# Kernel tuning notes

Measured on AMD Instinct MI355X. Metric: run time of the kernel, lower is better.

## Reference

```python
import jax, jax.numpy as jnp
import numpy as np

B, S, F, H = 2, 2048, 2048, 16
DH = F // H  # head_dim = 128
ROPE_BASE = 10000.0


def apply_rope(x, offset):
    # x: [B, S, H, Dh]; rotate-half RoPE per head with positions offset..offset+S-1
    d = x.shape[-1]
    pos = jnp.arange(x.shape[1], dtype=jnp.float32) + offset          # [S]
    inv_freq = 1.0 / (ROPE_BASE ** (jnp.arange(0, d, 2, dtype=jnp.float32) / d))  # [Dh/2]
    ang = pos[:, None] * inv_freq[None, :]                             # [S, Dh/2]
    cos = jnp.cos(ang)[None, :, None, :].astype(x.dtype)               # [1,S,1,Dh/2]
    sin = jnp.sin(ang)[None, :, None, :].astype(x.dtype)
    x1, x2 = x[..., : d // 2], x[..., d // 2 :]
    return jnp.concatenate([x1 * cos - x2 * sin, x1 * sin + x2 * cos], axis=-1)


def setup_inputs() -> dict:
    key = jax.random.key(0)
    k0, k1, k2, k3 = jax.random.split(key, 4)
    lecun = (1.0 / F) ** 0.5
    in_q = jax.random.normal(k0, (B, S, F), dtype=jnp.float32)
    Wq = jax.random.normal(k1, (F, H, DH), dtype=jnp.float32) * lecun
    Wk = jax.random.normal(k2, (F, H, DH), dtype=jnp.float32) * lecun
    Wv = jax.random.normal(k3, (F, H, DH), dtype=jnp.float32) * lecun
    bq = jnp.zeros((H, DH), dtype=jnp.float32)
    bk = jnp.zeros((H, DH), dtype=jnp.float32)
    bv = jnp.zeros((H, DH), dtype=jnp.float32)
    mask = jnp.tril(jnp.ones((S, S), dtype=bool))[None, None, :, :]  # causal [1,1,S,S]
    return {"in_q": in_q, "Wq": Wq, "bq": bq, "Wk": Wk, "bk": bk,
            "Wv": Wv, "bv": bv, "mask": mask, "offset": 0}


def reference(in_q, Wq, bq, Wk, bk, Wv, bv, mask, offset):
    # QKV projections: LinearGeneral [B,S,F] x [F,H,Dh] -> [B,S,H,Dh]
    q = jnp.einsum("bsf,fhd->bshd", in_q, Wq) + bq
    k = jnp.einsum("bsf,fhd->bshd", in_q, Wk) + bk
    v = jnp.einsum("bsf,fhd->bshd", in_q, Wv) + bv
    # RoPE on q and k (merge/split-head reshape in original is a no-op on values)
    q = apply_rope(q, offset)
    k = apply_rope(k, offset)
    # dot-product attention
    scale = 1.0 / jnp.sqrt(jnp.asarray(DH, dtype=q.dtype))
    scores = jnp.einsum("bqhd,bkhd->bhqk", q, k) * scale   # [B,H,Sq,Skv]
    scores = jnp.where(mask, scores, jnp.finfo(scores.dtype).min)
    weights = jax.nn.softmax(scores, axis=-1)
    out = jnp.einsum("bhqk,bkhd->bqhd", weights, v)        # [B,S,H,Dh]
    return out.reshape(out.shape[0], out.shape[1], H * DH)  # merge heads
```

## Files before the change

kernel.cpp:

```cpp
#include <hip/hip_runtime.h>
#include <hip/hip_bf16.h>
#include <stdint.h>

#define NB 2
#define NS 2048
#define NFE 2048
#define NH 16
#define NDH 128

#define QSCALE (0.08838834764831845f * 1.4426950408889634f)

typedef __attribute__((ext_vector_type(4))) float f32x4;
typedef __attribute__((ext_vector_type(8))) __bf16 bf16x8;

__device__ __forceinline__ uint16_t f2bf(float f) {
  uint32_t u = __builtin_bit_cast(uint32_t, f);
  return (uint16_t)((u + 0x7fffu + ((u >> 16) & 1u)) >> 16);
}

__device__ __forceinline__ void gload_lds16(const void* g, void* l) {
  __builtin_amdgcn_global_load_lds((const __attribute__((address_space(1))) void*)g,
                                   (__attribute__((address_space(3))) void*)l,
                                   16, 0, 0);
}

#define MFMA16(a, b, c) __builtin_amdgcn_mfma_f32_16x16x32_bf16(a, b, c, 0, 0, 0)

__global__ void k_convert(const float* __restrict__ x, uint16_t* __restrict__ y,
                          float* __restrict__ cosT, float* __restrict__ sinT,
                          const int* __restrict__ offp) {
  int b = blockIdx.x;
  if (b < 8192) {
    int i = (b * 256 + threadIdx.x) * 4;
    float4 v = *(const float4*)(x + i);
    ushort4 o;
    o.x = f2bf(v.x); o.y = f2bf(v.y); o.z = f2bf(v.z); o.w = f2bf(v.w);
    *(ushort4*)(y + i) = o;
  } else {
    int tid = (b - 8192) * 256 + threadIdx.x;
    int s = tid >> 6, i = tid & 63;
    float off = (float)offp[0];
    float inv = expf(-((float)i / 64.0f) * logf(10000.0f));
    float ang = ((float)s + off) * inv;
    cosT[tid] = cosf(ang);
    sinT[tid] = sinf(ang);
  }
}

__global__ void k_wt(const float* __restrict__ Wq, const float* __restrict__ Wk,
                     const float* __restrict__ Wv, uint16_t* __restrict__ Wt) {
  int which = blockIdx.z;
  const float* Wsrc = (which == 0) ? Wq : ((which == 1) ? Wk : Wv);
  int k0 = blockIdx.x * 64, n0 = blockIdx.y * 64;
  __shared__ uint16_t tile[64][65];
  int t = threadIdx.x;
#pragma unroll
  for (int it = 0; it < 4; ++it) {
    int vec = t + it * 256;
    int r = vec >> 4, c4 = vec & 15;
    float4 v = *(const float4*)&Wsrc[(size_t)(k0 + r) * NFE + n0 + c4 * 4];
    tile[r][c4 * 4 + 0] = f2bf(v.x);
    tile[r][c4 * 4 + 1] = f2bf(v.y);
    tile[r][c4 * 4 + 2] = f2bf(v.z);
    tile[r][c4 * 4 + 3] = f2bf(v.w);
  }
  __syncthreads();
#pragma unroll
  for (int it = 0; it < 4; ++it) {
    int vec = t + it * 256;
    int r = vec >> 4, c4 = vec & 15;
    ushort4 o;
    o.x = tile[c4 * 4 + 0][r];
    o.y = tile[c4 * 4 + 1][r];
    o.z = tile[c4 * 4 + 2][r];
    o.w = tile[c4 * 4 + 3][r];
    *(ushort4*)&Wt[(size_t)which * NFE * NFE + (size_t)(n0 + r) * NFE + k0 + c4 * 4] = o;
  }
}

__global__ __launch_bounds__(256, 2) void k_gemm_qkv(
    const uint16_t* __restrict__ A, const uint16_t* __restrict__ Wt,
    const float* __restrict__ bq, const float* __restrict__ bk, const float* __restrict__ bv,
    const float* __restrict__ cosT, const float* __restrict__ sinT,
    uint16_t* __restrict__ qws, uint16_t* __restrict__ kws, uint16_t* __restrict__ vws) {
  __shared__ alignas(16) uint16_t Asm[128 * 64];
  __shared__ alignas(16) uint16_t Bsm[128 * 64];
  int mt = blockIdx.x;
  int nt = blockIdx.y;
  int which = nt >> 4, h = nt & 15;
  const uint16_t* Bsrc = Wt + (size_t)which * NFE * NFE + (size_t)h * NDH * NFE;
  const uint16_t* Arow = A + (size_t)mt * 128 * NFE;
  int t = threadIdx.x, w = t >> 6, l = t & 63;
  int g = l >> 4, c = l & 15;

  f32x4 acc[2][8];
#pragma unroll
  for (int m = 0; m < 2; ++m)
#pragma unroll
    for (int n = 0; n < 8; ++n) acc[m][n] = (f32x4){0.f, 0.f, 0.f, 0.f};

  for (int kt = 0; kt < NFE / 64; ++kt) {
    int k0 = kt * 64;
#pragma unroll
    for (int cc = 0; cc < 4; ++cc) {
      int flat = cc * 256 + t;
      int row = flat >> 3, sub = flat & 7;
      int scol = ((sub ^ (row & 7)) << 3) + k0;
      gload_lds16(&Arow[(size_t)row * NFE + scol], (char*)Asm + flat * 16);
    }
#pragma unroll
    for (int cc = 0; cc < 4; ++cc) {
      int flat = cc * 256 + t;
      int row = flat >> 3, sub = flat & 7;
      int scol = ((sub ^ (row & 7)) << 3) + k0;
      gload_lds16(&Bsrc[(size_t)row * NFE + scol], (char*)Bsm + flat * 16);
    }
    __syncthreads();
#pragma unroll
    for (int ks = 0; ks < 2; ++ks) {
      bf16x8 af[2];
#pragma unroll
      for (int m = 0; m < 2; ++m) {
        int row = w * 32 + m * 16 + c;
        int kb = ((ks * 32 + g * 8) * 2) ^ ((row & 7) << 4);
        af[m] = *(const bf16x8*)((const char*)Asm + row * 128 + kb);
      }
#pragma unroll
      for (int nf = 0; nf < 8; ++nf) {
        int row = nf * 16 + c;
        int kb = ((ks * 32 + g * 8) * 2) ^ ((row & 7) << 4);
        bf16x8 bfr = *(const bf16x8*)((const char*)Bsm + row * 128 + kb);
        acc[0][nf] = MFMA16(af[0], bfr, acc[0][nf]);
        acc[1][nf] = MFMA16(af[1], bfr, acc[1][nf]);
      }
    }
    __syncthreads();
  }

  const float* bias = (which == 0) ? bq : ((which == 1) ? bk : bv);
  uint16_t* outp = (which == 0) ? qws : ((which == 1) ? kws : vws);
  float scl = (which == 0) ? QSCALE : 1.0f;
  int mbase = mt * 128 + w * 32;
  if (which < 2) {
#pragma unroll
    for (int m = 0; m < 2; ++m)
#pragma unroll
      for (int nf = 0; nf < 4; ++nf) {
        int i = nf * 16 + c;
        float b1 = bias[h * NDH + i], b2 = bias[h * NDH + 64 + i];
#pragma unroll
        for (int j = 0; j < 4; ++j) {
          int r = mbase + m * 16 + g * 4 + j;
          int bb = r >> 11, s = r & (NS - 1);
          float cs = cosT[(s << 6) + i], sn = sinT[(s << 6) + i];
          float x1 = acc[m][nf][j] + b1;
          float x2 = acc[m][nf + 4][j] + b2;
          uint16_t* op = outp + ((size_t)(bb * NH + h) * NS + s) * NDH;
          op[i] = f2bf((x1 * cs - x2 * sn) * scl);
          op[64 + i] = f2bf((x1 * sn + x2 * cs) * scl);
        }
      }
  } else {
#pragma unroll
    for (int m = 0; m < 2; ++m)
#pragma unroll
      for (int nf = 0; nf < 8; ++nf) {
        int d = nf * 16 + c;
        float bv_ = bias[h * NDH + d];
#pragma unroll
        for (int j = 0; j < 4; ++j) {
          int r = mbase + m * 16 + g * 4 + j;
          int bb = r >> 11, s = r & (NS - 1);
          outp[((size_t)(bb * NH + h) * NS + s) * NDH + d] = f2bf(acc[m][nf][j] + bv_);
        }
      }
  }
}

__global__ void k_vt(const uint16_t* __restrict__ v, uint16_t* __restrict__ vt) {
  int bh = blockIdx.z;
  int s0 = blockIdx.x * 64, d0 = blockIdx.y * 64;
  __shared__ uint16_t tile[64][65];
  int t = threadIdx.x;
#pragma unroll
  for (int it = 0; it < 4; ++it) {
    int vec = t + it * 256;
    int r = vec >> 4, c4 = vec & 15;
    ushort4 x = *(const ushort4*)&v[((size_t)bh * NS + s0 + r) * NDH + d0 + c4 * 4];
    tile[r][c4 * 4 + 0] = x.x;
    tile[r][c4 * 4 + 1] = x.y;
    tile[r][c4 * 4 + 2] = x.z;
    tile[r][c4 * 4 + 3] = x.w;
  }
  __syncthreads();
#pragma unroll
  for (int it = 0; it < 4; ++it) {
    int vec = t + it * 256;
    int r = vec >> 4, c4 = vec & 15;
    ushort4 o;
    o.x = tile[c4 * 4 + 0][r];
    o.y = tile[c4 * 4 + 1][r];
    o.z = tile[c4 * 4 + 2][r];
    o.w = tile[c4 * 4 + 3][r];
    *(ushort4*)&vt[((size_t)bh * NDH + d0 + r) * NS + s0 + c4 * 4] = o;
  }
}

__global__ __launch_bounds__(256, 4) void k_attn(
    const uint16_t* __restrict__ qws, const uint16_t* __restrict__ kws,
    const uint16_t* __restrict__ vtws, float* __restrict__ out) {
  __shared__ alignas(16) uint16_t Ksm[2][64 * 128];
  __shared__ alignas(16) uint16_t Vsm[2][128 * 64];
  __shared__ alignas(16) uint16_t Psm[4][16 * 64];

  int bh = blockIdx.x;
  int t = threadIdx.x, w = t >> 6, l = t & 63;
  int g = l >> 4, c = l & 15;
  int bb = bh >> 4, h = bh & 15;

  const uint16_t* Qp = qws + (size_t)bh * NS * NDH;
  const uint16_t* Kp = kws + (size_t)bh * NS * NDH;
  const uint16_t* Vp = vtws + (size_t)bh * NDH * NS;

#define STAGE(bb_, kt_)                                                            \
  do {                                                                             \
    _Pragma("unroll") for (int cc = 0; cc < 4; ++cc) {                             \
      int flat = cc * 256 + t;                                                     \
      int row = flat >> 4, sub = flat & 15;                                        \
      int scol = ((sub ^ (row & 7)) << 3);                                         \
      gload_lds16(&Kp[(size_t)((kt_) * 64 + row) * NDH + scol],                    \
                  (char*)Ksm[bb_] + flat * 16);                                    \
    }                                                                              \
    _Pragma("unroll") for (int cc = 0; cc < 4; ++cc) {                             \
      int flat = cc * 256 + t;                                                     \
      int row = flat >> 3, sub = flat & 7;                                         \
      int scol = ((sub ^ (row & 7)) << 3);                                         \
      gload_lds16(&Vp[(size_t)row * NS + (kt_) * 64 + scol],                       \
                  (char*)Vsm[bb_] + flat * 16);                                    \
    }                                                                              \
  } while (0)

  for (int pass = 0; pass < 2; ++pass) {
    int y64 = pass ? (31 - blockIdx.y) : blockIdx.y;
    int q0 = y64 * 64;
    int r = q0 + w * 16 + c;

    bf16x8 qf[4];
#pragma unroll
    for (int kk = 0; kk < 4; ++kk)
      qf[kk] = *(const bf16x8*)&Qp[(size_t)r * NDH + kk * 32 + g * 8];

    f32x4 acc_o[8];
    float mreg = -1e30f, lreg = 0.f;
#pragma unroll
    for (int n = 0; n < 8; ++n) acc_o[n] = (f32x4){0.f, 0.f, 0.f, 0.f};

    int nkt = y64 + 1;
    STAGE(0, 0);
    __syncthreads();

    for (int kt = 0; kt < nkt; ++kt) {
      int cur = kt & 1;
      if (kt + 1 < nkt) STAGE(cur ^ 1, kt + 1);

      f32x4 sacc[4];
#pragma unroll
      for (int nf = 0; nf < 4; ++nf) sacc[nf] = (f32x4){0.f, 0.f, 0.f, 0.f};
#pragma unroll
      for (int kk = 0; kk < 4; ++kk) {
#pragma unroll
        for (int nf = 0; nf < 4; ++nf) {
          int row = nf * 16 + c;
          int kb = ((kk * 32 + g * 8) * 2) ^ ((row & 7) << 4);
          bf16x8 kfr = *(const bf16x8*)((const char*)Ksm[cur] + row * 256 + kb);
          sacc[nf] = MFMA16(kfr, qf[kk], sacc[nf]);
        }
      }

      if (kt == y64) {
#pragma unroll
        for (int nf = 0; nf < 4; ++nf)
#pragma unroll
          for (int j = 0; j < 4; ++j) {
            int kv = kt * 64 + nf * 16 + g * 4 + j;
            if (kv > r) sacc[nf][j] = -1e30f;
          }
      }

      float mx = -1e30f;
#pragma unroll
      for (int nf = 0; nf < 4; ++nf)
        mx = fmaxf(mx, fmaxf(fmaxf(sacc[nf][0], sacc[nf][1]),
                             fmaxf(sacc[nf][2], sacc[nf][3])));
      mx = fmaxf(mx, __shfl_xor(mx, 16));
      mx = fmaxf(mx, __shfl_xor(mx, 32));

      float mnew = mreg;
      if (!__all(mx <= mreg + 8.0f)) {
        mnew = fmaxf(mreg, mx);
        float alpha = exp2f(mreg - mnew);
        mreg = mnew;
        lreg *= alpha;
#pragma unroll
        for (int j = 0; j < 4; ++j) {
          float aj = __shfl(alpha, (l & 48) + g * 4 + j);
#pragma unroll
          for (int nf = 0; nf < 8; ++nf) acc_o[nf][j] *= aj;
        }
      }

      float rs = 0.f;
#pragma unroll
      for (int nf = 0; nf < 4; ++nf)
#pragma unroll
        for (int j = 0; j < 4; ++j) {
          float p = exp2f(sacc[nf][j] - mnew);
          sacc[nf][j] = p;
          rs += p;
        }
      rs += __shfl_xor(rs, 16);
      rs += __shfl_xor(rs, 32);
      lreg += rs;

#pragma unroll
      for (int nf = 0; nf < 4; ++nf) {
        uint32_t pk0 = (uint32_t)f2bf(sacc[nf][0]) | ((uint32_t)f2bf(sacc[nf][1]) << 16);
        uint32_t pk1 = (uint32_t)f2bf(sacc[nf][2]) | ((uint32_t)f2bf(sacc[nf][3]) << 16);
        int colb = (nf * 16 + g * 4) * 2;
        char* base = (char*)Psm[w] + c * 128;
        *(uint32_t*)(base + (colb ^ ((c & 7) << 4))) = pk0;
        *(uint32_t*)(base + ((colb + 4) ^ ((c & 7) << 4))) = pk1;
      }

#pragma unroll
      for (int kk2 = 0; kk2 < 2; ++kk2) {
        int prow = c;
        int pkb = ((kk2 * 32 + g * 8) * 2) ^ ((prow & 7) << 4);
        bf16x8 pf = *(const bf16x8*)((const char*)Psm[w] + prow * 128 + pkb);
#pragma unroll
        for (int nf = 0; nf < 8; ++nf) {
          int row = nf * 16 + c;
          int kb = ((kk2 * 32 + g * 8) * 2) ^ ((row & 7) << 4);
          bf16x8 vf = *(const bf16x8*)((const char*)Vsm[cur] + row * 128 + kb);
          acc_o[nf] = MFMA16(pf, vf, acc_o[nf]);
        }
      }
      __syncthreads();
    }

#pragma unroll
    for (int j = 0; j < 4; ++j) {
      float lj = __shfl(lreg, (l & 48) + g * 4 + j);
      float inv = 1.0f / lj;
      int s = q0 + w * 16 + g * 4 + j;
      float* op = out + ((size_t)(bb * NS + s)) * NFE + h * NDH;
#pragma unroll
      for (int nf = 0; nf < 8; ++nf) op[nf * 16 + c] = acc_o[nf][j] * inv;
    }
  }
#undef STAGE
}

extern "C" void kernel_launch(void* const* d_in, const int* in_sizes, int n_in,
                              void* d_out, int out_size, void* d_ws, size_t ws_size,
                              hipStream_t stream) {
  const float* in_q = (const float*)d_in[0];
  const float* Wq = (const float*)d_in[1];
  const float* bq = (const float*)d_in[2];
  const float* Wk = (const float*)d_in[3];
  const float* bk = (const float*)d_in[4];
  const float* Wv = (const float*)d_in[5];
  const float* bv = (const float*)d_in[6];
  const int* offp = (const int*)d_in[8];
  float* out = (float*)d_out;

  char* ws = (char*)d_ws;
  const size_t SZ_AQ = (size_t)4096 * 2048 * 2;
  const size_t SZ_WT = (size_t)3 * 2048 * 2048 * 2;
  const size_t SZ_TAB = (size_t)2048 * 64 * 4;
  const size_t SZ_QKV = (size_t)32 * 2048 * 128 * 2;
  uint16_t* Aq = (uint16_t*)(ws);
  uint16_t* Wt = (uint16_t*)(ws + SZ_AQ);
  float* cosT = (float*)(ws + SZ_AQ + SZ_WT);
  float* sinT = (float*)(ws + SZ_AQ + SZ_WT + SZ_TAB);
  uint16_t* qws = (uint16_t*)(ws + SZ_AQ + SZ_WT + 2 * SZ_TAB);
  uint16_t* kws = (uint16_t*)(ws + SZ_AQ + SZ_WT + 2 * SZ_TAB + SZ_QKV);
  uint16_t* vws = (uint16_t*)(ws + SZ_AQ + SZ_WT + 2 * SZ_TAB + 2 * SZ_QKV);
  uint16_t* vtws = (uint16_t*)(ws + SZ_AQ + SZ_WT + 2 * SZ_TAB + 3 * SZ_QKV);

  k_convert<<<8704, 256, 0, stream>>>(in_q, Aq, cosT, sinT, offp);
  k_wt<<<dim3(32, 32, 3), 256, 0, stream>>>(Wq, Wk, Wv, Wt);
  k_gemm_qkv<<<dim3(32, 48), 256, 0, stream>>>(Aq, Wt, bq, bk, bv, cosT, sinT, qws, kws, vws);
  k_vt<<<dim3(32, 2, 32), 256, 0, stream>>>(vws, vtws);
  k_attn<<<dim3(32, 16), 256, 0, stream>>>(qws, kws, vtws, out);
}
```

Measured before the change: 200.8 us.

## Fuse weight transpose into prep kernel and write V transposed from GEMM epilogue

Merges the input conversion, RoPE table and weight-transpose kernels into one launch. The V projection epilogue now stages its tile in LDS with a swizzle and writes V already transposed, which removes the separate V transpose kernel and its extra global round trip. This cuts two launches and one read-and-write pass over V, at the cost of an extra LDS stage and sync in the GEMM epilogue for the V blocks.

```diff
diff --git a/kernel.cpp b/kernel.cpp
--- a/kernel.cpp
+++ b/kernel.cpp
@@ -26,55 +26,55 @@
 
 #define MFMA16(a, b, c) __builtin_amdgcn_mfma_f32_16x16x32_bf16(a, b, c, 0, 0, 0)
 
-__global__ void k_convert(const float* __restrict__ x, uint16_t* __restrict__ y,
-                          float* __restrict__ cosT, float* __restrict__ sinT,
-                          const int* __restrict__ offp) {
+__global__ void k_prep(const float* __restrict__ x, uint16_t* __restrict__ y,
+                       float* __restrict__ cosT, float* __restrict__ sinT,
+                       const int* __restrict__ offp,
+                       const float* __restrict__ Wq, const float* __restrict__ Wk,
+                       const float* __restrict__ Wv, uint16_t* __restrict__ Wt) {
+  __shared__ uint16_t tile[64][65];
   int b = blockIdx.x;
+  int t = threadIdx.x;
   if (b < 8192) {
-    int i = (b * 256 + threadIdx.x) * 4;
+    int i = (b * 256 + t) * 4;
     float4 v = *(const float4*)(x + i);
     ushort4 o;
     o.x = f2bf(v.x); o.y = f2bf(v.y); o.z = f2bf(v.z); o.w = f2bf(v.w);
     *(ushort4*)(y + i) = o;
-  } else {
-    int tid = (b - 8192) * 256 + threadIdx.x;
+  } else if (b < 8704) {
+    int tid = (b - 8192) * 256 + t;
     int s = tid >> 6, i = tid & 63;
     float off = (float)offp[0];
     float inv = expf(-((float)i / 64.0f) * logf(10000.0f));
     float ang = ((float)s + off) * inv;
     cosT[tid] = cosf(ang);
     sinT[tid] = sinf(ang);
-  }
-}
-
-__global__ void k_wt(const float* __restrict__ Wq, const float* __restrict__ Wk,
-                     const float* __restrict__ Wv, uint16_t* __restrict__ Wt) {
-  int which = blockIdx.z;
-  const float* Wsrc = (which == 0) ? Wq : ((which == 1) ? Wk : Wv);
-  int k0 = blockIdx.x * 64, n0 = blockIdx.y * 64;
-  __shared__ uint16_t tile[64][65];
-  int t = threadIdx.x;
-#pragma unroll
-  for (int it = 0; it < 4; ++it) {
-    int vec = t + it * 256;
-    int r = vec >> 4, c4 = vec & 15;
-    float4 v = *(const float4*)&Wsrc[(size_t)(k0 + r) * NFE + n0 + c4 * 4];
-    tile[r][c4 * 4 + 0] = f2bf(v.x);
-    tile[r][c4 * 4 + 1] = f2bf(v.y);
-    tile[r][c4 * 4 + 2] = f2bf(v.z);
-    tile[r][c4 * 4 + 3] = f2bf(v.w);
-  }
-  __syncthreads();
-#pragma unroll
-  for (int it = 0; it < 4; ++it) {
-    int vec = t + it * 256;
-    int r = vec >> 4, c4 = vec & 15;
-    ushort4 o;
-    o.x = tile[c4 * 4 + 0][r];
-    o.y = tile[c4 * 4 + 1][r];
-    o.z = tile[c4 * 4 + 2][r];
-    o.w = tile[c4 * 4 + 3][r];
-    *(ushort4*)&Wt[(size_t)which * NFE * NFE + (size_t)(n0 + r) * NFE + k0 + c4 * 4] = o;
+  } else {
+    int idx = b - 8704;
+    int which = idx >> 10, rem = idx & 1023;
+    int k0 = (rem & 31) * 64, n0 = (rem >> 5) * 64;
+    const float* Wsrc = (which == 0) ? Wq : ((which == 1) ? Wk : Wv);
+#pragma unroll
+    for (int it = 0; it < 4; ++it) {
+      int vec = t + it * 256;
+      int r = vec >> 4, c4 = vec & 15;
+      float4 v = *(const float4*)&Wsrc[(size_t)(k0 + r) * NFE + n0 + c4 * 4];
+      tile[r][c4 * 4 + 0] = f2bf(v.x);
+      tile[r][c4 * 4 + 1] = f2bf(v.y);
+      tile[r][c4 * 4 + 2] = f2bf(v.z);
+      tile[r][c4 * 4 + 3] = f2bf(v.w);
+    }
+    __syncthreads();
+#pragma unroll
+    for (int it = 0; it < 4; ++it) {
+      int vec = t + it * 256;
+      int r = vec >> 4, c4 = vec & 15;
+      ushort4 o;
+      o.x = tile[c4 * 4 + 0][r];
+      o.y = tile[c4 * 4 + 1][r];
+      o.z = tile[c4 * 4 + 2][r];
+      o.w = tile[c4 * 4 + 3][r];
+      *(ushort4*)&Wt[(size_t)which * NFE * NFE + (size_t)(n0 + r) * NFE + k0 + c4 * 4] = o;
+    }
   }
 }
 
@@ -82,9 +82,10 @@
     const uint16_t* __restrict__ A, const uint16_t* __restrict__ Wt,
     const float* __restrict__ bq, const float* __restrict__ bk, const float* __restrict__ bv,
     const float* __restrict__ cosT, const float* __restrict__ sinT,
-    uint16_t* __restrict__ qws, uint16_t* __restrict__ kws, uint16_t* __restrict__ vws) {
-  __shared__ alignas(16) uint16_t Asm[128 * 64];
-  __shared__ alignas(16) uint16_t Bsm[128 * 64];
+    uint16_t* __restrict__ qws, uint16_t* __restrict__ kws, uint16_t* __restrict__ vtws) {
+  __shared__ alignas(16) uint16_t SM[2 * 128 * 64];
+  uint16_t* Asm = SM;
+  uint16_t* Bsm = SM + 8192;
   int mt = blockIdx.x;
   int nt = blockIdx.y;
   int which = nt >> 4, h = nt & 15;
@@ -137,11 +138,11 @@
     __syncthreads();
   }
 
-  const float* bias = (which == 0) ? bq : ((which == 1) ? bk : bv);
-  uint16_t* outp = (which == 0) ? qws : ((which == 1) ? kws : vws);
-  float scl = (which == 0) ? QSCALE : 1.0f;
   int mbase = mt * 128 + w * 32;
   if (which < 2) {
+    const float* bias = (which == 0) ? bq : bk;
+    uint16_t* outp = (which == 0) ? qws : kws;
+    float scl = (which == 0) ? QSCALE : 1.0f;
 #pragma unroll
     for (int m = 0; m < 2; ++m)
 #pragma unroll
@@ -166,43 +167,29 @@
 #pragma unroll
       for (int nf = 0; nf < 8; ++nf) {
         int d = nf * 16 + c;
-        float bv_ = bias[h * NDH + d];
-#pragma unroll
-        for (int j = 0; j < 4; ++j) {
-          int r = mbase + m * 16 + g * 4 + j;
-          int bb = r >> 11, s = r & (NS - 1);
-          outp[((size_t)(bb * NH + h) * NS + s) * NDH + d] = f2bf(acc[m][nf][j] + bv_);
-        }
-      }
-  }
-}
-
-__global__ void k_vt(const uint16_t* __restrict__ v, uint16_t* __restrict__ vt) {
-  int bh = blockIdx.z;
-  int s0 = blockIdx.x * 64, d0 = blockIdx.y * 64;
-  __shared__ uint16_t tile[64][65];
-  int t = threadIdx.x;
-#pragma unroll
-  for (int it = 0; it < 4; ++it) {
-    int vec = t + it * 256;
-    int r = vec >> 4, c4 = vec & 15;
-    ushort4 x = *(const ushort4*)&v[((size_t)bh * NS + s0 + r) * NDH + d0 + c4 * 4];
-    tile[r][c4 * 4 + 0] = x.x;
-    tile[r][c4 * 4 + 1] = x.y;
-    tile[r][c4 * 4 + 2] = x.z;
-    tile[r][c4 * 4 + 3] = x.w;
-  }
-  __syncthreads();
-#pragma unroll
-  for (int it = 0; it < 4; ++it) {
-    int vec = t + it * 256;
-    int r = vec >> 4, c4 = vec & 15;
-    ushort4 o;
-    o.x = tile[c4 * 4 + 0][r];
-    o.y = tile[c4 * 4 + 1][r];
-    o.z = tile[c4 * 4 + 2][r];
-    o.w = tile[c4 * 4 + 3][r];
-    *(ushort4*)&vt[((size_t)bh * NDH + d0 + r) * NS + s0 + c4 * 4] = o;
+        float bv_ = bv[h * NDH + d];
+#pragma unroll
+        for (int j = 0; j < 4; j += 2) {
+          int sp = w * 32 + m * 16 + g * 4 + j;
+          int idx = d * 128 + (sp ^ ((d & 7) << 3));
+          uint32_t pk = (uint32_t)f2bf(acc[m][nf][j] + bv_) |
+                        ((uint32_t)f2bf(acc[m][nf][j + 1] + bv_) << 16);
+          *(uint32_t*)((char*)SM + (size_t)idx * 2) = pk;
+        }
+      }
+    __syncthreads();
+    int bb = mt >> 4;
+    int s_base = (mt & 15) * 128;
+    uint16_t* vtb = vtws + (size_t)(bb * NH + h) * NDH * NS;
+#pragma unroll
+    for (int it = 0; it < 8; ++it) {
+      int flat = it * 256 + t;
+      int d = flat >> 4, chunk = flat & 15;
+      int s0 = chunk * 8;
+      int idx = d * 128 + (s0 ^ ((d & 7) << 3));
+      bf16x8 vv = *(const bf16x8*)((const char*)SM + (size_t)idx * 2);
+      *(bf16x8*)(vtb + (size_t)d * NS + s_base + s0) = vv;
+    }
   }
 }
 
@@ -385,12 +372,9 @@
   float* sinT = (float*)(ws + SZ_AQ + SZ_WT + SZ_TAB);
   uint16_t* qws = (uint16_t*)(ws + SZ_AQ + SZ_WT + 2 * SZ_TAB);
   uint16_t* kws = (uint16_t*)(ws + SZ_AQ + SZ_WT + 2 * SZ_TAB + SZ_QKV);
-  uint16_t* vws = (uint16_t*)(ws + SZ_AQ + SZ_WT + 2 * SZ_TAB + 2 * SZ_QKV);
-  uint16_t* vtws = (uint16_t*)(ws + SZ_AQ + SZ_WT + 2 * SZ_TAB + 3 * SZ_QKV);
-
-  k_convert<<<8704, 256, 0, stream>>>(in_q, Aq, cosT, sinT, offp);
-  k_wt<<<dim3(32, 32, 3), 256, 0, stream>>>(Wq, Wk, Wv, Wt);
-  k_gemm_qkv<<<dim3(32, 48), 256, 0, stream>>>(Aq, Wt, bq, bk, bv, cosT, sinT, qws, kws, vws);
-  k_vt<<<dim3(32, 2, 32), 256, 0, stream>>>(vws, vtws);
+  uint16_t* vtws = (uint16_t*)(ws + SZ_AQ + SZ_WT + 2 * SZ_TAB + 2 * SZ_QKV);
+
+  k_prep<<<11776, 256, 0, stream>>>(in_q, Aq, cosT, sinT, offp, Wq, Wk, Wv, Wt);
+  k_gemm_qkv<<<dim3(32, 48), 256, 0, stream>>>(Aq, Wt, bq, bk, bv, cosT, sinT, qws, kws, vtws);
   k_attn<<<dim3(32, 16), 256, 0, stream>>>(qws, kws, vtws, out);
 }
```

After: 190.7 us. -5.1%, faster.
